# Kernel optimization log

Hardware: AMD Instinct MI355X
Metric: run time of the kernel (lower is better)

Reference implementation:

```python
import jax, jax.numpy as jnp
import numpy as np

H, D = 4, 32            # heads, per-head out_channels (hidden_channels)
N, E = 50000, 800000    # nodes, edges
CIN, COUT = 256, 128    # conv in_channels, module out_channels


def setup_inputs() -> dict:
    key = jax.random.key(0)
    ks = jax.random.split(key, 20)
    w = lambda k, shape: (jax.random.normal(k, shape, jnp.float32) * 0.05)
    x = jax.random.normal(ks[0], (N, COUT), jnp.float32)
    t = jax.random.uniform(ks[1], (N, 1), dtype=jnp.float32)
    edge_index = jax.random.randint(ks[2], (2, E), 0, N)
    edge_weight = jax.random.uniform(ks[3], (E, 1), dtype=jnp.float32)
    return {
        'x': x, 't': t, 'edge_index': edge_index, 'edge_weight': edge_weight,
        # TransformerConv params (PyG): lin_query/key/value: Linear(CIN, H*D)
        'Wq': w(ks[4], (CIN, H * D)), 'bq': w(ks[5], (H * D,)),
        'Wk': w(ks[6], (CIN, H * D)), 'bk': w(ks[7], (H * D,)),
        'Wv': w(ks[8], (CIN, H * D)), 'bv': w(ks[9], (H * D,)),
        # lin_edge: Linear(edge_dim=1, H*D)
        'We': w(ks[10], (1, H * D)), 'be': w(ks[11], (H * D,)),
        # lin_skip (root weight, concat=False): Linear(CIN, D)
        'Wskip': w(ks[12], (CIN, D)), 'bskip': w(ks[13], (D,)),
        # mlp: Linear(D, 2*COUT) + tanh
        'Wmlp': w(ks[14], (D, 2 * COUT)), 'bmlp': w(ks[15], (2 * COUT,)),
    }


def _transformer_conv(y, edge_index, edge_attr, Wq, bq, Wk, bk, Wv, bv, We, be, Wskip, bskip):
    n = y.shape[0]
    q = (y @ Wq + bq).reshape(n, H, D)
    k = (y @ Wk + bk).reshape(n, H, D)
    v = (y @ Wv + bv).reshape(n, H, D)
    e = (edge_attr @ We + be).reshape(-1, H, D)          # [E,H,D]
    src, dst = edge_index[0], edge_index[1]
    k_e = k[src] + e                                     # edge-gathered keys
    alpha = jnp.einsum('ehd,ehd->eh', q[dst], k_e) / jnp.sqrt(jnp.float32(D))
    # segment softmax over incoming edges of each dst node
    m = jax.ops.segment_max(alpha, dst, num_segments=n)
    m = jnp.where(jnp.isfinite(m), m, 0.0)
    p = jnp.exp(alpha - m[dst])
    denom = jax.ops.segment_sum(p, dst, num_segments=n)
    attn = p / (denom[dst] + 1e-16)                      # [E,H]
    msg = (v[src] + e) * attn[..., None]                 # [E,H,D]
    agg = jax.ops.segment_sum(msg, dst, num_segments=n)  # [N,H,D]
    # concat=False -> mean over heads, plus root/skip term
    return agg.mean(axis=1) + y @ Wskip + bskip          # [N,D]


def reference(x, t, edge_index, edge_weight, Wq, bq, Wk, bk, Wv, bv, We, be, Wskip, bskip, Wmlp, bmlp):
    y0 = jnp.concatenate([x, x * t], axis=-1)            # [N, 2*COUT] = [N, CIN]
    y = _transformer_conv(y0, edge_index, edge_weight, Wq, bq, Wk, bk, Wv, bv, We, be, Wskip, bskip)
    y = jnp.tanh(y)                                      # activation after conv
    y = jnp.tanh(y @ Wmlp + bmlp)                        # mlp -> [N, 2*COUT]
    scale = y[:, :COUT]
    shift = y[:, COUT:]
    return x * scale + shift                             # FiLM conditioning (skip: identity x)
```

## Files before the change

kernel.cpp:

```cpp
#include <hip/hip_runtime.h>
#include <hip/hip_bf16.h>

#define NNODES 50000
#define NPAD   50048
#define NEDGES 800000
#define CAP 64
#define RSQRT_D 0.17677669529663687f

typedef short short8 __attribute__((ext_vector_type(8)));
typedef float f32x4 __attribute__((ext_vector_type(4)));

__device__ inline unsigned short f2bf(float f) {
    union { float f; unsigned u; } v; v.f = f;
    unsigned r = (v.u + 0x7fff + ((v.u >> 16) & 1)) >> 16;
    return (unsigned short)r;
}
__device__ inline float bf2f(unsigned short u) {
    union { unsigned u; float f; } v; v.u = ((unsigned)u) << 16;
    return v.f;
}
__device__ inline float bflo(unsigned u) {
    union { unsigned u; float f; } v; v.u = u << 16; return v.f;
}
__device__ inline float bfhi(unsigned u) {
    union { unsigned u; float f; } v; v.u = u & 0xffff0000u; return v.f;
}
__device__ inline float fast_tanh(float v) {
    const float e = __expf(2.0f * v);
    return 1.0f - 2.0f * __builtin_amdgcn_rcpf(e + 1.0f);
}

__global__ __launch_bounds__(256) void prep_w(
    const float* __restrict__ Wq, const float* __restrict__ bq,
    const float* __restrict__ Wk, const float* __restrict__ bk,
    const float* __restrict__ Wv, const float* __restrict__ bv,
    const float* __restrict__ Wskip, const float* __restrict__ bskip,
    unsigned short* __restrict__ Wtf, float* __restrict__ biascat)
{
    const int col = blockIdx.x;
    const int k = threadIdx.x;
    float v; float b;
    if (col < 128)      { v = Wq[k * 128 + col];          b = bq[col]; }
    else if (col < 256) { v = Wk[k * 128 + col - 128];    b = bk[col - 128]; }
    else if (col < 384) { v = Wv[k * 128 + col - 256];    b = bv[col - 256]; }
    else                { v = Wskip[k * 32 + col - 384];  b = bskip[col - 384]; }
    const int ct = col >> 4, c16 = col & 15;
    const int kt = k >> 5, quad = (k >> 3) & 3, j = k & 7;
    Wtf[(size_t)(ct * 32 + kt * 4 + quad) * 128 + c16 * 8 + j] = f2bf(v);
    if (k == 0) biascat[col] = b;
}

__global__ __launch_bounds__(256) void pack_a(
    const float* __restrict__ x, const float* __restrict__ t,
    unsigned short* __restrict__ y0f)
{
    const int gid = blockIdx.x * 256 + threadIdx.x;
    const int row = gid >> 5;
    const int oct = gid & 31;
    short8 out = {0, 0, 0, 0, 0, 0, 0, 0};
    if (row < NNODES) {
        const int kb = oct * 8;
        const int kx = (kb < 128) ? kb : (kb - 128);
        const float* xr = x + (size_t)row * 128 + kx;
        float4 f0 = *(const float4*)xr;
        float4 f1 = *(const float4*)(xr + 4);
        if (kb >= 128) {
            const float tv = t[row];
            f0.x *= tv; f0.y *= tv; f0.z *= tv; f0.w *= tv;
            f1.x *= tv; f1.y *= tv; f1.z *= tv; f1.w *= tv;
        }
        out[0] = (short)f2bf(f0.x); out[1] = (short)f2bf(f0.y);
        out[2] = (short)f2bf(f0.z); out[3] = (short)f2bf(f0.w);
        out[4] = (short)f2bf(f1.x); out[5] = (short)f2bf(f1.y);
        out[6] = (short)f2bf(f1.z); out[7] = (short)f2bf(f1.w);
    }
    *(short8*)(y0f + (size_t)((row >> 4) * 32 + oct) * 128 + (row & 15) * 8) = out;
}

#define LOADW(buf, ct) do {                                                    \
    _Pragma("unroll")                                                          \
    for (int kt_ = 0; kt_ < 8; ++kt_)                                          \
        buf[kt_] = *(const short8*)(Wtf + (size_t)((ct) * 32 + kt_ * 4 + quad) * 128 + l16 * 8); \
} while (0)

#define DOTILE(buf, ct) do {                                                   \
    f32x4 acc0 = {0.f, 0.f, 0.f, 0.f}, acc1 = {0.f, 0.f, 0.f, 0.f};            \
    _Pragma("unroll")                                                          \
    for (int kt_ = 0; kt_ < 8; ++kt_) {                                        \
        acc0 = __builtin_amdgcn_mfma_f32_16x16x32_bf16(buf[kt_], b0[kt_], acc0, 0, 0, 0); \
        acc1 = __builtin_amdgcn_mfma_f32_16x16x32_bf16(buf[kt_], b1[kt_], acc1, 0, 0, 0); \
    }                                                                          \
    const int cb_ = (ct) * 16 + quad * 4;                                      \
    const float4 bias_ = *(const float4*)(biascat + cb_);                      \
    _Pragma("unroll")                                                          \
    for (int s_ = 0; s_ < 2; ++s_) {                                           \
        const int m_ = n0 + s_ * 16 + l16;                                     \
        if (m_ < NNODES) {                                                     \
            const f32x4 a_ = s_ ? acc1 : acc0;                                 \
            const float v0_ = a_[0] + bias_.x, v1_ = a_[1] + bias_.y;          \
            const float v2_ = a_[2] + bias_.z, v3_ = a_[3] + bias_.w;          \
            if ((ct) < 24) {                                                   \
                uint2 pk_;                                                     \
                pk_.x = (unsigned)f2bf(v0_) | ((unsigned)f2bf(v1_) << 16);     \
                pk_.y = (unsigned)f2bf(v2_) | ((unsigned)f2bf(v3_) << 16);     \
                if ((ct) < 8)                                                  \
                    *(uint2*)(Qb + (size_t)m_ * 128 + cb_) = pk_;              \
                else                                                           \
                    *(uint2*)(KVb + (size_t)m_ * 256 + (cb_ - 128)) = pk_;     \
            } else {                                                           \
                *(float4*)(S + (size_t)m_ * 32 + (cb_ - 384)) =                \
                    make_float4(v0_, v1_, v2_, v3_);                           \
            }                                                                  \
        }                                                                      \
    }                                                                          \
} while (0)

__global__ __launch_bounds__(256) void gemm_mfma(
    const unsigned short* __restrict__ y0f,
    const unsigned short* __restrict__ Wtf,
    const float* __restrict__ biascat,
    unsigned short* __restrict__ Qb, unsigned short* __restrict__ KVb,
    float* __restrict__ S)
{
    const int tid = threadIdx.x;
    const int wave = tid >> 6;
    const int lane = tid & 63;
    const int l16 = lane & 15;
    const int quad = lane >> 4;

    const int n0 = blockIdx.x * 128 + wave * 32;
    const int mt0 = n0 >> 4;
    const int by = blockIdx.y;
    const int ct0 = by * 7 - ((by >= 2) ? (by - 2) : 0);
    const int nct = (by < 2) ? 7 : 6;
    const int ctEnd = ct0 + nct;

    short8 b0[8], b1[8];
    #pragma unroll
    for (int kt = 0; kt < 8; ++kt) {
        b0[kt] = *(const short8*)(y0f + (size_t)((mt0 + 0) * 32 + kt * 4 + quad) * 128 + l16 * 8);
        b1[kt] = *(const short8*)(y0f + (size_t)((mt0 + 1) * 32 + kt * 4 + quad) * 128 + l16 * 8);
    }

    short8 wa[8], wb[8];
    LOADW(wa, ct0);
    for (int ct = ct0; ct < ctEnd; ct += 2) {
        if (ct + 1 < ctEnd) LOADW(wb, ct + 1);
        DOTILE(wa, ct);
        if (ct + 1 < ctEnd) {
            if (ct + 2 < ctEnd) LOADW(wa, ct + 2);
            DOTILE(wb, ct + 1);
        }
    }
}

__global__ __launch_bounds__(256) void scatter_fill(
    const int* __restrict__ ei, const float* __restrict__ ew,
    int* __restrict__ cnt, int2* __restrict__ einfo)
{
    const int e = blockIdx.x * 256 + threadIdx.x;
    if (e >= NEDGES) return;
    const int src = ei[e];
    const int dst = ei[NEDGES + e];
    const int pos = atomicAdd(&cnt[dst], 1);
    if (pos < CAP) {
        int2 v; v.x = src; v.y = __float_as_int(ew[e]);
        einfo[(size_t)dst * CAP + pos] = v;
    }
}

__global__ __launch_bounds__(256) void agg_pass(
    const int* __restrict__ cnt, const int2* __restrict__ einfo,
    const float* __restrict__ We, const float* __restrict__ be,
    const unsigned short* __restrict__ Qb, const unsigned short* __restrict__ KVb,
    float* __restrict__ G)
{
    const int tid = threadIdx.x;
    const int node = blockIdx.x * 4 + (tid >> 6);
    if (node >= NNODES) return;
    const int l = tid & 63;
    const int slot = l >> 4;
    const int q = l & 15;

    const uint4 qu = *(const uint4*)(Qb + (size_t)node * 128 + q * 8);
    float qv[8];
    qv[0] = bflo(qu.x); qv[1] = bfhi(qu.x);
    qv[2] = bflo(qu.y); qv[3] = bfhi(qu.y);
    qv[4] = bflo(qu.z); qv[5] = bfhi(qu.z);
    qv[6] = bflo(qu.w); qv[7] = bfhi(qu.w);

    const float4 weA = *(const float4*)(We + q * 8);
    const float4 weB = *(const float4*)(We + q * 8 + 4);
    const float4 beA = *(const float4*)(be + q * 8);
    const float4 beB = *(const float4*)(be + q * 8 + 4);

    float pw = qv[0]*weA.x + qv[1]*weA.y + qv[2]*weA.z + qv[3]*weA.w
             + qv[4]*weB.x + qv[5]*weB.y + qv[6]*weB.z + qv[7]*weB.w;
    float pb = qv[0]*beA.x + qv[1]*beA.y + qv[2]*beA.z + qv[3]*beA.w
             + qv[4]*beB.x + qv[5]*beB.y + qv[6]*beB.z + qv[7]*beB.w;
    pw += __shfl_xor(pw, 1); pb += __shfl_xor(pb, 1);
    pw += __shfl_xor(pw, 2); pb += __shfl_xor(pb, 2);
    const float qWeS = pw * RSQRT_D;
    const float qbeS = pb * RSQRT_D;

    const int deg = min(cnt[node], CAP);
    const int2* ep = einfo + (size_t)node * CAP;

    int2 eall = make_int2(0, 0);
    const int loadN = min(CAP, ((deg + 3) & ~3) + 4);
    if (l < loadN) eall = ep[l];

    float a[8] = {0.f, 0.f, 0.f, 0.f, 0.f, 0.f, 0.f, 0.f};
    float sp = 0.f, spw = 0.f;

    const char* kvb = (const char*)KVb;
    const unsigned qoff = (unsigned)(q * 16);

    int ecx = __shfl(eall.x, slot);
    int ecy = __shfl(eall.y, slot);
    bool vc = (slot < deg);
    {
        const unsigned off = (((unsigned)(vc ? ecx : 0)) << 9) + qoff;
        uint4 kw = *(const uint4*)(kvb + off);
        uint4 vw = *(const uint4*)(kvb + off + 256);
        float wc = __int_as_float(ecy);

        for (int jj = 0; jj < deg; jj += 4) {
            const int nidx = (jj + 4 + slot) & 63;
            const int enx = __shfl(eall.x, nidx);
            const int eny = __shfl(eall.y, nidx);
            const bool vn = (jj + 4 + slot < deg);
            const unsigned offn = (((unsigned)(vn ? enx : 0)) << 9) + qoff;
            const uint4 kwn = *(const uint4*)(kvb + offn);
            const uint4 vwn = *(const uint4*)(kvb + offn + 256);
            const float wn = __int_as_float(eny);

            float d = qv[0]*bflo(kw.x) + qv[1]*bfhi(kw.x)
                    + qv[2]*bflo(kw.y) + qv[3]*bfhi(kw.y)
                    + qv[4]*bflo(kw.z) + qv[5]*bfhi(kw.z)
                    + qv[6]*bflo(kw.w) + qv[7]*bfhi(kw.w);
            d += __shfl_xor(d, 1);
            d += __shfl_xor(d, 2);
            float p = __expf(d * RSQRT_D + wc * qWeS + qbeS);
            p = vc ? p : 0.f;
            sp += p; spw += p * wc;
            a[0] += p * bflo(vw.x); a[1] += p * bfhi(vw.x);
            a[2] += p * bflo(vw.y); a[3] += p * bfhi(vw.y);
            a[4] += p * bflo(vw.z); a[5] += p * bfhi(vw.z);
            a[6] += p * bflo(vw.w); a[7] += p * bfhi(vw.w);

            kw = kwn; vw = vwn; wc = wn; vc = vn;
        }
    }

    sp  += __shfl_xor(sp, 16);  sp  += __shfl_xor(sp, 32);
    spw += __shfl_xor(spw, 16); spw += __shfl_xor(spw, 32);
    #pragma unroll
    for (int i = 0; i < 8; ++i) {
        a[i] += __shfl_xor(a[i], 16);
        a[i] += __shfl_xor(a[i], 32);
    }

    const float inv = 1.f / (sp + 1e-16f);
    a[0] = (a[0] + spw*weA.x + sp*beA.x) * inv;
    a[1] = (a[1] + spw*weA.y + sp*beA.y) * inv;
    a[2] = (a[2] + spw*weA.z + sp*beA.z) * inv;
    a[3] = (a[3] + spw*weA.w + sp*beA.w) * inv;
    a[4] = (a[4] + spw*weB.x + sp*beB.x) * inv;
    a[5] = (a[5] + spw*weB.y + sp*beB.y) * inv;
    a[6] = (a[6] + spw*weB.z + sp*beB.z) * inv;
    a[7] = (a[7] + spw*weB.w + sp*beB.w) * inv;

    #pragma unroll
    for (int i = 0; i < 8; ++i) {
        a[i] += __shfl_xor(a[i], 4);
        a[i] += __shfl_xor(a[i], 8);
    }

    if (l < 4) {
        *(float4*)(G + (size_t)node * 32 + q * 8) =
            make_float4(a[0]*0.25f, a[1]*0.25f, a[2]*0.25f, a[3]*0.25f);
        *(float4*)(G + (size_t)node * 32 + q * 8 + 4) =
            make_float4(a[4]*0.25f, a[5]*0.25f, a[6]*0.25f, a[7]*0.25f);
    }
}

__global__ __launch_bounds__(256, 4) void node_pass(
    const float* __restrict__ x,
    const float* __restrict__ G, const float* __restrict__ S,
    const float* __restrict__ Wmlp, const float* __restrict__ bmlp,
    float* __restrict__ out)
{
    __shared__ float yl[64 * 32];

    const int tid = threadIdx.x;
    const int c = tid & 127;
    const int half = tid >> 7;

    float w1[32], w2[32];
    #pragma unroll
    for (int d = 0; d < 32; ++d) {
        w1[d] = Wmlp[d * 256 + c];
        w2[d] = Wmlp[d * 256 + c + 128];
    }
    const float b1 = bmlp[c];
    const float b2 = bmlp[c + 128];

    const int n0 = blockIdx.x * 64;

    for (int i4 = tid; i4 < 512; i4 += 256) {
        const int n = n0 + (i4 >> 3);
        const int d0 = (i4 & 7) * 4;
        float4 yv = make_float4(0.f, 0.f, 0.f, 0.f);
        if (n < NNODES) {
            const float4 gv = *(const float4*)(G + (size_t)n * 32 + d0);
            const float4 sv = *(const float4*)(S + (size_t)n * 32 + d0);
            yv.x = fast_tanh(gv.x + sv.x);
            yv.y = fast_tanh(gv.y + sv.y);
            yv.z = fast_tanh(gv.z + sv.z);
            yv.w = fast_tanh(gv.w + sv.w);
        }
        *(float4*)&yl[i4 * 4] = yv;
    }
    __syncthreads();

    for (int k = 0; k < 32; ++k) {
        const int nl = 2 * k + half;
        const int n = n0 + nl;
        if (n >= NNODES) continue;

        const float4* yr = (const float4*)&yl[nl * 32];
        float s1 = b1, s2 = b2;
        #pragma unroll
        for (int d8 = 0; d8 < 8; ++d8) {
            const float4 y4 = yr[d8];
            s1 = fmaf(y4.x, w1[d8 * 4 + 0], s1);
            s2 = fmaf(y4.x, w2[d8 * 4 + 0], s2);
            s1 = fmaf(y4.y, w1[d8 * 4 + 1], s1);
            s2 = fmaf(y4.y, w2[d8 * 4 + 1], s2);
            s1 = fmaf(y4.z, w1[d8 * 4 + 2], s1);
            s2 = fmaf(y4.z, w2[d8 * 4 + 2], s2);
            s1 = fmaf(y4.w, w1[d8 * 4 + 3], s1);
            s2 = fmaf(y4.w, w2[d8 * 4 + 3], s2);
        }
        const float z1 = fast_tanh(s1);
        const float z2 = fast_tanh(s2);
        out[(size_t)n * 128 + c] = fmaf(x[(size_t)n * 128 + c], z1, z2);
    }
}

extern "C" void kernel_launch(void* const* d_in, const int* in_sizes, int n_in,
                              void* d_out, int out_size, void* d_ws, size_t ws_size,
                              hipStream_t stream) {
    const float* x     = (const float*)d_in[0];
    const float* t     = (const float*)d_in[1];
    const int*   ei    = (const int*)  d_in[2];
    const float* ew    = (const float*)d_in[3];
    const float* Wq    = (const float*)d_in[4];
    const float* bq    = (const float*)d_in[5];
    const float* Wk    = (const float*)d_in[6];
    const float* bk    = (const float*)d_in[7];
    const float* Wv    = (const float*)d_in[8];
    const float* bv    = (const float*)d_in[9];
    const float* We    = (const float*)d_in[10];
    const float* be    = (const float*)d_in[11];
    const float* Wskip = (const float*)d_in[12];
    const float* bskip = (const float*)d_in[13];
    const float* Wmlp  = (const float*)d_in[14];
    const float* bmlp  = (const float*)d_in[15];

    char* p = (char*)d_ws;
    unsigned short* Qb  = (unsigned short*)p; p += (size_t)NNODES * 128 * 2;
    unsigned short* KVb = (unsigned short*)p; p += (size_t)NNODES * 256 * 2;
    float* S       = (float*)p; p += (size_t)NNODES * 32 * 4;
    float* G       = (float*)p; p += (size_t)NNODES * 32 * 4;
    unsigned short* Wtf = (unsigned short*)p; p += 416 * 256 * 2;
    float* biascat = (float*)p; p += 416 * 4;
    unsigned short* y0f = (unsigned short*)p; p += (size_t)NPAD * 256 * 2;
    int2* einfo    = (int2*)p;  p += (size_t)NNODES * CAP * 8;
    int* cnt       = (int*)p;   p += NNODES * 4;

    hipMemsetAsync(cnt, 0, (size_t)NNODES * sizeof(int), stream);

    prep_w<<<416, 256, 0, stream>>>(Wq, bq, Wk, bk, Wv, bv, Wskip, bskip,
                                    Wtf, biascat);

    pack_a<<<(NPAD * 32) / 256, 256, 0, stream>>>(x, t, y0f);

    scatter_fill<<<NEDGES / 256, 256, 0, stream>>>(ei, ew, cnt, einfo);

    dim3 gg(NPAD / 128, 4);
    gemm_mfma<<<gg, 256, 0, stream>>>(y0f, Wtf, biascat, Qb, KVb, S);

    agg_pass<<<(NNODES + 3) / 4, 256, 0, stream>>>(cnt, einfo, We, be, Qb, KVb, G);

    node_pass<<<(NNODES + 63) / 64, 256, 0, stream>>>(x, G, S, Wmlp, bmlp,
                                                      (float*)d_out);
}
```

Measured before the change: 285.7 us.

## Fuse edge scatter into GEMM launch and deepen agg gather prefetch to four stages

Merges the scatter_fill kernel into the MFMA GEMM launch by interleaving blocks: two scatter blocks for every GEMM block. This lets the atomic-bound scatter overlap with the compute-bound GEMM and removes one launch. Separately, the attention aggregation loop now keeps four edge groups of K/V gathers in flight instead of one, to hide gather latency. The deeper prefetch raises register use and issues extra masked loads past the node's degree.

```diff
diff --git a/kernel.cpp b/kernel.cpp
--- a/kernel.cpp
+++ b/kernel.cpp
@@ -6,6 +6,9 @@
 #define NEDGES 800000
 #define CAP 64
 #define RSQRT_D 0.17677669529663687f
+
+#define SCAT_BLOCKS 3125
+#define GEMM_BLOCKS 1564
 
 typedef short short8 __attribute__((ext_vector_type(8)));
 typedef float f32x4 __attribute__((ext_vector_type(4)));
@@ -115,22 +118,45 @@
     }                                                                          \
 } while (0)
 
-__global__ __launch_bounds__(256) void gemm_mfma(
+__global__ __launch_bounds__(256) void gemm_scatter(
     const unsigned short* __restrict__ y0f,
     const unsigned short* __restrict__ Wtf,
     const float* __restrict__ biascat,
     unsigned short* __restrict__ Qb, unsigned short* __restrict__ KVb,
-    float* __restrict__ S)
+    float* __restrict__ S,
+    const int* __restrict__ ei, const float* __restrict__ ew,
+    int* __restrict__ cnt, int2* __restrict__ einfo)
 {
+    const int b = blockIdx.x;
+    const int group = b / 3;
+    const int r = b - group * 3;
+
+    if (r < 2) {
+        const int sb = group * 2 + r;
+        if (sb >= SCAT_BLOCKS) return;
+        const int e = sb * 256 + threadIdx.x;
+        const int src = ei[e];
+        const int dst = ei[NEDGES + e];
+        const int pos = atomicAdd(&cnt[dst], 1);
+        if (pos < CAP) {
+            int2 v; v.x = src; v.y = __float_as_int(ew[e]);
+            einfo[(size_t)dst * CAP + pos] = v;
+        }
+        return;
+    }
+
+    const int g = group;
+    const int bx = g % 391;
+    const int by = g / 391;
+
     const int tid = threadIdx.x;
     const int wave = tid >> 6;
     const int lane = tid & 63;
     const int l16 = lane & 15;
     const int quad = lane >> 4;
 
-    const int n0 = blockIdx.x * 128 + wave * 32;
+    const int n0 = bx * 128 + wave * 32;
     const int mt0 = n0 >> 4;
-    const int by = blockIdx.y;
     const int ct0 = by * 7 - ((by >= 2) ? (by - 2) : 0);
     const int nct = (by < 2) ? 7 : 6;
     const int ctEnd = ct0 + nct;
@@ -154,20 +180,32 @@
     }
 }
 
-__global__ __launch_bounds__(256) void scatter_fill(
-    const int* __restrict__ ei, const float* __restrict__ ew,
-    int* __restrict__ cnt, int2* __restrict__ einfo)
-{
-    const int e = blockIdx.x * 256 + threadIdx.x;
-    if (e >= NEDGES) return;
-    const int src = ei[e];
-    const int dst = ei[NEDGES + e];
-    const int pos = atomicAdd(&cnt[dst], 1);
-    if (pos < CAP) {
-        int2 v; v.x = src; v.y = __float_as_int(ew[e]);
-        einfo[(size_t)dst * CAP + pos] = v;
-    }
-}
+#define AGG_ISSUE(K, V, W, F, base) do {                                       \
+    const int idx_ = ((base) + slot) & 63;                                     \
+    const int ex_ = __shfl(eall.x, idx_);                                      \
+    const int ey_ = __shfl(eall.y, idx_);                                      \
+    F = ((base) + slot) < deg;                                                 \
+    const unsigned off_ = (((unsigned)(F ? ex_ : 0)) << 9) + qoff;             \
+    K = *(const uint4*)(kvb + off_);                                           \
+    V = *(const uint4*)(kvb + off_ + 256);                                     \
+    W = __int_as_float(ey_);                                                   \
+} while (0)
+
+#define AGG_COMPUTE(K, V, W, F) do {                                           \
+    float d_ = qv[0]*bflo(K.x) + qv[1]*bfhi(K.x)                               \
+             + qv[2]*bflo(K.y) + qv[3]*bfhi(K.y)                               \
+             + qv[4]*bflo(K.z) + qv[5]*bfhi(K.z)                               \
+             + qv[6]*bflo(K.w) + qv[7]*bfhi(K.w);                              \
+    d_ += __shfl_xor(d_, 1);                                                   \
+    d_ += __shfl_xor(d_, 2);                                                   \
+    float p_ = __expf(d_ * RSQRT_D + W * qWeS + qbeS);                         \
+    p_ = F ? p_ : 0.f;                                                         \
+    sp += p_; spw += p_ * W;                                                   \
+    a[0] += p_ * bflo(V.x); a[1] += p_ * bfhi(V.x);                            \
+    a[2] += p_ * bflo(V.y); a[3] += p_ * bfhi(V.y);                            \
+    a[4] += p_ * bflo(V.z); a[5] += p_ * bfhi(V.z);                            \
+    a[6] += p_ * bflo(V.w); a[7] += p_ * bfhi(V.w);                            \
+} while (0)
 
 __global__ __launch_bounds__(256) void agg_pass(
     const int* __restrict__ cnt, const int2* __restrict__ einfo,
@@ -216,41 +254,23 @@
     const char* kvb = (const char*)KVb;
     const unsigned qoff = (unsigned)(q * 16);
 
-    int ecx = __shfl(eall.x, slot);
-    int ecy = __shfl(eall.y, slot);
-    bool vc = (slot < deg);
-    {
-        const unsigned off = (((unsigned)(vc ? ecx : 0)) << 9) + qoff;
-        uint4 kw = *(const uint4*)(kvb + off);
-        uint4 vw = *(const uint4*)(kvb + off + 256);
-        float wc = __int_as_float(ecy);
-
-        for (int jj = 0; jj < deg; jj += 4) {
-            const int nidx = (jj + 4 + slot) & 63;
-            const int enx = __shfl(eall.x, nidx);
-            const int eny = __shfl(eall.y, nidx);
-            const bool vn = (jj + 4 + slot < deg);
-            const unsigned offn = (((unsigned)(vn ? enx : 0)) << 9) + qoff;
-            const uint4 kwn = *(const uint4*)(kvb + offn);
-            const uint4 vwn = *(const uint4*)(kvb + offn + 256);
-            const float wn = __int_as_float(eny);
-
-            float d = qv[0]*bflo(kw.x) + qv[1]*bfhi(kw.x)
-                    + qv[2]*bflo(kw.y) + qv[3]*bfhi(kw.y)
-                    + qv[4]*bflo(kw.z) + qv[5]*bfhi(kw.z)
-                    + qv[6]*bflo(kw.w) + qv[7]*bfhi(kw.w);
-            d += __shfl_xor(d, 1);
-            d += __shfl_xor(d, 2);
-            float p = __expf(d * RSQRT_D + wc * qWeS + qbeS);
-            p = vc ? p : 0.f;
-            sp += p; spw += p * wc;
-            a[0] += p * bflo(vw.x); a[1] += p * bfhi(vw.x);
-            a[2] += p * bflo(vw.y); a[3] += p * bfhi(vw.y);
-            a[4] += p * bflo(vw.z); a[5] += p * bfhi(vw.z);
-            a[6] += p * bflo(vw.w); a[7] += p * bfhi(vw.w);
-
-            kw = kwn; vw = vwn; wc = wn; vc = vn;
-        }
+    uint4 k0, v0, k1, v1, k2, v2, k3, v3;
+    float w0, w1, w2, w3;
+    bool f0, f1, f2, f3;
+    AGG_ISSUE(k0, v0, w0, f0, 0);
+    AGG_ISSUE(k1, v1, w1, f1, 4);
+    AGG_ISSUE(k2, v2, w2, f2, 8);
+    AGG_ISSUE(k3, v3, w3, f3, 12);
+
+    for (int jj = 0; jj < deg; jj += 16) {
+        AGG_COMPUTE(k0, v0, w0, f0);
+        AGG_ISSUE(k0, v0, w0, f0, jj + 16);
+        AGG_COMPUTE(k1, v1, w1, f1);
+        AGG_ISSUE(k1, v1, w1, f1, jj + 20);
+        AGG_COMPUTE(k2, v2, w2, f2);
+        AGG_ISSUE(k2, v2, w2, f2, jj + 24);
+        AGG_COMPUTE(k3, v3, w3, f3);
+        AGG_ISSUE(k3, v3, w3, f3, jj + 28);
     }
 
     sp  += __shfl_xor(sp, 16);  sp  += __shfl_xor(sp, 32);
@@ -387,10 +407,8 @@
 
     pack_a<<<(NPAD * 32) / 256, 256, 0, stream>>>(x, t, y0f);
 
-    scatter_fill<<<NEDGES / 256, 256, 0, stream>>>(ei, ew, cnt, einfo);
-
-    dim3 gg(NPAD / 128, 4);
-    gemm_mfma<<<gg, 256, 0, stream>>>(y0f, Wtf, biascat, Qb, KVb, S);
+    gemm_scatter<<<GEMM_BLOCKS * 3, 256, 0, stream>>>(
+        y0f, Wtf, biascat, Qb, KVb, S, ei, ew, cnt, einfo);
 
     agg_pass<<<(NNODES + 3) / 4, 256, 0, stream>>>(cnt, einfo, We, be, Qb, KVb, G);
 
```

Result: faster. 262.6 us (-8.1%).

## Fuse edge scatter into GEMM kernel via interleaved block roles

Applied to the files above, without the earlier changes.

Merges the scatter_fill and gemm_mfma launches into one kernel. Blocks are interleaved so one of every three runs the GEMM and the other two each bucket 1024 edges, four per thread, which lets memory-bound atomics overlap with MFMA work. Each GEMM block now covers all 26 column tiles for its 128 rows instead of splitting them over a 4-wide grid.y. In exchange there are fewer GEMM blocks with longer per-block work, and the two roles compete for the same compute units.

```diff
diff --git a/kernel.cpp b/kernel.cpp
--- a/kernel.cpp
+++ b/kernel.cpp
@@ -6,6 +6,9 @@
 #define NEDGES 800000
 #define CAP 64
 #define RSQRT_D 0.17677669529663687f
+
+#define GEMM_BLOCKS 391
+#define SCAT_BLOCKS 782
 
 typedef short short8 __attribute__((ext_vector_type(8)));
 typedef float f32x4 __attribute__((ext_vector_type(4)));
@@ -115,25 +118,63 @@
     }                                                                          \
 } while (0)
 
-__global__ __launch_bounds__(256) void gemm_mfma(
+__global__ __launch_bounds__(256) void gemm_scatter(
     const unsigned short* __restrict__ y0f,
     const unsigned short* __restrict__ Wtf,
     const float* __restrict__ biascat,
     unsigned short* __restrict__ Qb, unsigned short* __restrict__ KVb,
-    float* __restrict__ S)
+    float* __restrict__ S,
+    const int* __restrict__ ei, const float* __restrict__ ew,
+    int* __restrict__ cnt, int2* __restrict__ einfo)
 {
+    const int b = blockIdx.x;
+    const int g = b / 3;
+    const int r = b - g * 3;
+
+    if (r) {
+        const int sb = g * 2 + (r - 1);
+        const int e0 = sb * 1024 + threadIdx.x;
+        const int e1 = e0 + 256, e2 = e0 + 512, e3 = e0 + 768;
+        const bool m0 = e0 < NEDGES, m1 = e1 < NEDGES,
+                   m2 = e2 < NEDGES, m3 = e3 < NEDGES;
+        int s0 = 0, s1 = 0, s2 = 0, s3 = 0;
+        int d0 = 0, d1 = 0, d2 = 0, d3 = 0;
+        float w0 = 0.f, w1 = 0.f, w2 = 0.f, w3 = 0.f;
+        if (m0) { s0 = ei[e0]; d0 = ei[NEDGES + e0]; w0 = ew[e0]; }
+        if (m1) { s1 = ei[e1]; d1 = ei[NEDGES + e1]; w1 = ew[e1]; }
+        if (m2) { s2 = ei[e2]; d2 = ei[NEDGES + e2]; w2 = ew[e2]; }
+        if (m3) { s3 = ei[e3]; d3 = ei[NEDGES + e3]; w3 = ew[e3]; }
+        if (m0) {
+            const int pos = atomicAdd(&cnt[d0], 1);
+            if (pos < CAP) { int2 v; v.x = s0; v.y = __float_as_int(w0);
+                             einfo[(size_t)d0 * CAP + pos] = v; }
+        }
+        if (m1) {
+            const int pos = atomicAdd(&cnt[d1], 1);
+            if (pos < CAP) { int2 v; v.x = s1; v.y = __float_as_int(w1);
+                             einfo[(size_t)d1 * CAP + pos] = v; }
+        }
+        if (m2) {
+            const int pos = atomicAdd(&cnt[d2], 1);
+            if (pos < CAP) { int2 v; v.x = s2; v.y = __float_as_int(w2);
+                             einfo[(size_t)d2 * CAP + pos] = v; }
+        }
+        if (m3) {
+            const int pos = atomicAdd(&cnt[d3], 1);
+            if (pos < CAP) { int2 v; v.x = s3; v.y = __float_as_int(w3);
+                             einfo[(size_t)d3 * CAP + pos] = v; }
+        }
+        return;
+    }
+
     const int tid = threadIdx.x;
     const int wave = tid >> 6;
     const int lane = tid & 63;
     const int l16 = lane & 15;
     const int quad = lane >> 4;
 
-    const int n0 = blockIdx.x * 128 + wave * 32;
+    const int n0 = g * 128 + wave * 32;
     const int mt0 = n0 >> 4;
-    const int by = blockIdx.y;
-    const int ct0 = by * 7 - ((by >= 2) ? (by - 2) : 0);
-    const int nct = (by < 2) ? 7 : 6;
-    const int ctEnd = ct0 + nct;
 
     short8 b0[8], b1[8];
     #pragma unroll
@@ -143,29 +184,12 @@
     }
 
     short8 wa[8], wb[8];
-    LOADW(wa, ct0);
-    for (int ct = ct0; ct < ctEnd; ct += 2) {
-        if (ct + 1 < ctEnd) LOADW(wb, ct + 1);
+    LOADW(wa, 0);
+    for (int ct = 0; ct < 26; ct += 2) {
+        LOADW(wb, ct + 1);
         DOTILE(wa, ct);
-        if (ct + 1 < ctEnd) {
-            if (ct + 2 < ctEnd) LOADW(wa, ct + 2);
-            DOTILE(wb, ct + 1);
-        }
-    }
-}
-
-__global__ __launch_bounds__(256) void scatter_fill(
-    const int* __restrict__ ei, const float* __restrict__ ew,
-    int* __restrict__ cnt, int2* __restrict__ einfo)
-{
-    const int e = blockIdx.x * 256 + threadIdx.x;
-    if (e >= NEDGES) return;
-    const int src = ei[e];
-    const int dst = ei[NEDGES + e];
-    const int pos = atomicAdd(&cnt[dst], 1);
-    if (pos < CAP) {
-        int2 v; v.x = src; v.y = __float_as_int(ew[e]);
-        einfo[(size_t)dst * CAP + pos] = v;
+        if (ct + 2 < 26) LOADW(wa, ct + 2);
+        DOTILE(wb, ct + 1);
     }
 }
 
@@ -387,10 +411,8 @@
 
     pack_a<<<(NPAD * 32) / 256, 256, 0, stream>>>(x, t, y0f);
 
-    scatter_fill<<<NEDGES / 256, 256, 0, stream>>>(ei, ew, cnt, einfo);
-
-    dim3 gg(NPAD / 128, 4);
-    gemm_mfma<<<gg, 256, 0, stream>>>(y0f, Wtf, biascat, Qb, KVb, S);
+    gemm_scatter<<<GEMM_BLOCKS * 3, 256, 0, stream>>>(
+        y0f, Wtf, biascat, Qb, KVb, S, ei, ew, cnt, einfo);
 
     agg_pass<<<(NNODES + 3) / 4, 256, 0, stream>>>(cnt, einfo, We, be, Qb, KVb, G);
 
```

New measurement: 280.2 us. No clear change (-1.9%).
